# Kernel optimization log

Measured on AMD Instinct MI355X. Metric: run time of the kernel, lower is better.

Reference implementation:

```python
import jax, jax.numpy as jnp
import numpy as np

B, LINS, LHIS, LACT = 128, 64, 128, 32
VOCAB, ACTSZ = 2000, 100
INS_H, INS_E = 256, 128
ACT_E, ACT_IN, ACT_H = 128, 512, 512
POS_E, COL_E, COL_H = 32, 32, 32
ENV = 7 * (POS_E + COL_H)  # 448


def _lstm_cell(h, c, x, Wih, Whh, bih, bhh):
    # torch LSTM gate order: i, f, g, o
    g = x @ Wih.T + h @ Whh.T + bih + bhh
    i, f, gg, o = jnp.split(g, 4, axis=-1)
    c = jax.nn.sigmoid(f) * c + jax.nn.sigmoid(i) * jnp.tanh(gg)
    h = jax.nn.sigmoid(o) * jnp.tanh(c)
    return h, c


def _run_lstm(xs, Wih, Whh, bih, bhh):
    # xs: [T, N, D] -> hs: [T, N, H], zero initial state (torch default)
    N = xs.shape[1]
    H = Whh.shape[1]
    h0 = jnp.zeros((N, H), xs.dtype)

    def step(carry, x):
        h, c = carry
        h, c = _lstm_cell(h, c, x, Wih, Whh, bih, bhh)
        return (h, c), h

    _, hs = jax.lax.scan(step, (h0, h0), xs)
    return hs


def _bilstm_encode(tokens, emb, Wf, Uf, bf1, bf2, Wb, Ub, bb1, bb2):
    xs = emb[tokens].transpose(1, 0, 2)            # [L, B, E]
    hf = _run_lstm(xs, Wf, Uf, bf1, bf2)           # [L, B, H]
    hb = _run_lstm(xs[::-1], Wb, Ub, bb1, bb2)[::-1]
    return jnp.concatenate([hf, hb], -1).transpose(1, 0, 2)  # [B, L, 2H]


def _env_encode(tokens, color_emb, pos_emb, Wih, Whh, bih, bhh):
    # tokens: [B, 35] = 7 beakers x (id + 4 color slots)
    t = tokens.reshape(B, 7, 5)
    col = color_emb[t[:, :, 1:5]]                  # [B, 7, 4, COL_E]
    xs = col.reshape(B * 7, 4, COL_E).transpose(1, 0, 2)  # [4, B*7, COL_E]
    h_last = _run_lstm(xs, Wih, Whh, bih, bhh)[-1].reshape(B, 7, COL_H)
    pos = jnp.broadcast_to(pos_emb[None], (B, 7, POS_E))
    return jnp.concatenate([pos, h_last], -1).reshape(B, 7 * (POS_E + COL_H))


def _attend(A, H, q):
    # Faithful to attend(): scores = sum_k (H @ W)[b,l,k] * q[b,k]; softmax over l;
    # A = H @ W is query-independent so it is hoisted out of the decode loop.
    a = jax.nn.softmax(jnp.einsum('blk,bk->bl', A, q), axis=1)
    return jnp.einsum('bl,bld->bd', a, H)


def _forward(ins_tokens, his_tokens, actions, cur_env, ini_env,
             enc_emb, enc_Wih_f, enc_Whh_f, enc_bih_f, enc_bhh_f,
             enc_Wih_b, enc_Whh_b, enc_bih_b, enc_bhh_b,
             color_emb, pos_emb, ws_Wih, ws_Whh, ws_bih, ws_bhh,
             act_emb, W_c, W_p, W_sb1, W_sb2, W_sc1, W_sc2,
             Wbd_W, Wbd_b, dec_Wih, dec_Whh, dec_bih, dec_bhh,
             h2a_W, h2a_b, h0, c0):
    ins_enc = _bilstm_encode(ins_tokens, enc_emb, enc_Wih_f, enc_Whh_f, enc_bih_f,
                             enc_bhh_f, enc_Wih_b, enc_Whh_b, enc_bih_b, enc_bhh_b)
    his_enc = _bilstm_encode(his_tokens, enc_emb, enc_Wih_f, enc_Whh_f, enc_bih_f,
                             enc_bhh_f, enc_Wih_b, enc_Whh_b, enc_bih_b, enc_bhh_b)
    cur_ctx = _env_encode(cur_env, color_emb, pos_emb, ws_Wih, ws_Whh, ws_bih, ws_bhh)
    ini_ctx = _env_encode(ini_env, color_emb, pos_emb, ws_Wih, ws_Whh, ws_bih, ws_bhh)

    X = act_emb[actions]                            # [B, T, ACT_E]
    # Query-independent projections, hoisted out of the per-step loop (same math).
    A_c = jnp.einsum('bld,dk->blk', ins_enc, W_c)   # [B, LINS, ACT_H]
    A_p = jnp.einsum('bld,dk->blk', his_enc, W_p)   # [B, LHIS, ACT_H+2*INS_H]
    K = ACT_H + 2 * INS_H
    ini_rep = jnp.broadcast_to(ini_ctx[:, None, :], (B, LACT, ENV))
    cur_rep = jnp.broadcast_to(cur_ctx[:, None, :], (B, LACT, ENV))
    A_b1 = jnp.broadcast_to((ini_ctx @ W_sb1)[:, None, :], (B, LACT, K))
    A_b2 = jnp.broadcast_to((ini_ctx @ W_sb2)[:, None, :], (B, LACT, K))
    A_c1 = jnp.broadcast_to((cur_ctx @ W_sc1)[:, None, :], (B, LACT, K))
    A_c2 = jnp.broadcast_to((cur_ctx @ W_sc2)[:, None, :], (B, LACT, K))

    def step(carry, x_t):
        h, c = carry
        z_c = _attend(A_c, ins_enc, h)              # [B, 2*INS_H]
        q = jnp.concatenate([h, z_c], -1)           # [B, ACT_H+2*INS_H]
        z_p = _attend(A_p, his_enc, q)
        z_s1 = jnp.concatenate([_attend(A_b1, ini_rep, q),
                                _attend(A_b2, ini_rep, q)], -1)
        z_sk = jnp.concatenate([_attend(A_c1, cur_rep, q),
                                _attend(A_c2, cur_rep, q)], -1)
        hk1 = jnp.concatenate([z_c, z_p, z_s1, z_sk, x_t], -1)  # [B, 2944]
        hk = jnp.tanh(hk1 @ Wbd_W.T + Wbd_b)        # [B, ACT_IN]
        h, c = _lstm_cell(h, c, hk, dec_Wih, dec_Whh, dec_bih, dec_bhh)
        return (h, c), h

    _, outs = jax.lax.scan(step, (h0, c0), X.transpose(1, 0, 2))
    logits = outs.transpose(1, 0, 2) @ h2a_W.T + h2a_b  # [B, LACT, ACTSZ]
    return logits


def setup_inputs() -> dict:
    root = jax.random.key(0)
    ki = iter(jax.random.split(root, 40))

    def nrm(shape, s=0.05):
        return jax.random.normal(next(ki), shape, dtype=jnp.float32) * s

    inp = {}
    inp['ins_tokens'] = jax.random.randint(next(ki), (B, LINS), 0, VOCAB)
    inp['his_tokens'] = jax.random.randint(next(ki), (B, LHIS), 0, VOCAB)
    inp['actions'] = jax.random.randint(next(ki), (B, LACT), 0, ACTSZ)
    inp['cur_env'] = jax.random.randint(next(ki), (B, 35), 0, 7)
    inp['ini_env'] = jax.random.randint(next(ki), (B, 35), 0, 7)
    inp['enc_emb'] = nrm((VOCAB, INS_E))
    inp['enc_Wih_f'] = nrm((4 * INS_H, INS_E))
    inp['enc_Whh_f'] = nrm((4 * INS_H, INS_H))
    inp['enc_bih_f'] = nrm((4 * INS_H,))
    inp['enc_bhh_f'] = nrm((4 * INS_H,))
    inp['enc_Wih_b'] = nrm((4 * INS_H, INS_E))
    inp['enc_Whh_b'] = nrm((4 * INS_H, INS_H))
    inp['enc_bih_b'] = nrm((4 * INS_H,))
    inp['enc_bhh_b'] = nrm((4 * INS_H,))
    inp['color_emb'] = nrm((7, COL_E))
    inp['pos_emb'] = nrm((7, POS_E))
    inp['ws_Wih'] = nrm((4 * COL_H, COL_E))
    inp['ws_Whh'] = nrm((4 * COL_H, COL_H))
    inp['ws_bih'] = nrm((4 * COL_H,))
    inp['ws_bhh'] = nrm((4 * COL_H,))
    inp['act_emb'] = nrm((ACTSZ, ACT_E))
    inp['W_c'] = nrm((2 * INS_H, ACT_H))
    inp['W_p'] = nrm((2 * INS_H, 2 * INS_H + ACT_H))
    inp['W_sb1'] = nrm((ENV, ACT_H + 2 * INS_H))
    inp['W_sb2'] = nrm((ENV, ACT_H + 2 * INS_H))
    inp['W_sc1'] = nrm((ENV, ACT_H + 2 * INS_H))
    inp['W_sc2'] = nrm((ENV, ACT_H + 2 * INS_H))
    inp['Wbd_W'] = nrm((ACT_IN, 4 * ENV + 4 * INS_H + ACT_E))
    inp['Wbd_b'] = nrm((ACT_IN,))
    inp['dec_Wih'] = nrm((4 * ACT_H, ACT_IN))
    inp['dec_Whh'] = nrm((4 * ACT_H, ACT_H))
    inp['dec_bih'] = nrm((4 * ACT_H,))
    inp['dec_bhh'] = nrm((4 * ACT_H,))
    inp['h2a_W'] = nrm((ACTSZ, ACT_H))
    inp['h2a_b'] = nrm((ACTSZ,))
    inp['h0'] = nrm((B, ACT_H))
    inp['c0'] = nrm((B, ACT_H))
    return inp


def reference(ins_tokens, his_tokens, actions, cur_env, ini_env,
              enc_emb, enc_Wih_f, enc_Whh_f, enc_bih_f, enc_bhh_f,
              enc_Wih_b, enc_Whh_b, enc_bih_b, enc_bhh_b,
              color_emb, pos_emb, ws_Wih, ws_Whh, ws_bih, ws_bhh,
              act_emb, W_c, W_p, W_sb1, W_sb2, W_sc1, W_sc2,
              Wbd_W, Wbd_b, dec_Wih, dec_Whh, dec_bih, dec_bhh,
              h2a_W, h2a_b, h0, c0):
    return _forward(ins_tokens, his_tokens, actions, cur_env, ini_env,
                    enc_emb, enc_Wih_f, enc_Whh_f, enc_bih_f, enc_bhh_f,
                    enc_Wih_b, enc_Whh_b, enc_bih_b, enc_bhh_b,
                    color_emb, pos_emb, ws_Wih, ws_Whh, ws_bih, ws_bhh,
                    act_emb, W_c, W_p, W_sb1, W_sb2, W_sc1, W_sc2,
                    Wbd_W, Wbd_b, dec_Wih, dec_Whh, dec_bih, dec_bhh,
                    h2a_W, h2a_b, h0, c0)
```

## Files before the change

### kernel.cpp

```cpp
#include <hip/hip_runtime.h>


typedef unsigned short u16;
typedef __attribute__((ext_vector_type(8))) short bf16x8;
typedef __attribute__((ext_vector_type(4))) float f32x4;

#define DEVFN static __device__ __forceinline__

DEVFN float bf2f(u16 u) {
  unsigned int x = ((unsigned int)u) << 16;
  float f; __builtin_memcpy(&f, &x, 4); return f;
}
DEVFN u16 f2bf(float f) {
  unsigned int x; __builtin_memcpy(&x, &f, 4);
  x = (x + 0x7fffu + ((x >> 16) & 1u)) >> 16;
  return (u16)x;
}
DEVFN float sigf(float x) { return 1.f / (1.f + __expf(-x)); }
DEVFN bf16x8 load8(const u16* p) { return *(const bf16x8*)p; }
DEVFN int clampi(int v, int lo, int hi) { return v < lo ? lo : (v > hi ? hi : v); }

struct GemmArgs {
  const u16* A; int lda; int M;
  const u16* W; int ldw; int N; int K;
  void* out; int ldc;
  const float* bias;
  const float* hk_base; const float* proj_act; const int* actions; int t;
};

template <int EPI>
__global__ __launch_bounds__(256) void gemm_k(GemmArgs g) {
  int lane = threadIdx.x & 63;
  int wave = threadIdx.x >> 6;
  int col = lane & 15, q = lane >> 4;
  int m0 = blockIdx.x * 64 + (wave >> 1) * 32;
  int n0 = blockIdx.y * 64 + (wave & 1) * 32;
  f32x4 acc[2][2] = {};
  int rA[2] = { m0 + col, m0 + 16 + col };
  int rB[2] = { n0 + col, n0 + 16 + col };
  bool gA[2] = { rA[0] < g.M, rA[1] < g.M };
  bool gB[2] = { rB[0] < g.N, rB[1] < g.N };
  const u16* pA[2]; const u16* pB[2];
#pragma unroll
  for (int i = 0; i < 2; i++) {
    pA[i] = g.A + (size_t)(gA[i] ? rA[i] : 0) * g.lda + q * 8;
    pB[i] = g.W + (size_t)(gB[i] ? rB[i] : 0) * g.ldw + q * 8;
  }
  bf16x8 zf = {0,0,0,0,0,0,0,0};
  for (int k = 0; k < g.K; k += 32) {
    bf16x8 a0 = gA[0] ? load8(pA[0] + k) : zf;
    bf16x8 a1 = gA[1] ? load8(pA[1] + k) : zf;
    bf16x8 b0 = gB[0] ? load8(pB[0] + k) : zf;
    bf16x8 b1 = gB[1] ? load8(pB[1] + k) : zf;
    acc[0][0] = __builtin_amdgcn_mfma_f32_16x16x32_bf16(a0, b0, acc[0][0], 0, 0, 0);
    acc[0][1] = __builtin_amdgcn_mfma_f32_16x16x32_bf16(a0, b1, acc[0][1], 0, 0, 0);
    acc[1][0] = __builtin_amdgcn_mfma_f32_16x16x32_bf16(a1, b0, acc[1][0], 0, 0, 0);
    acc[1][1] = __builtin_amdgcn_mfma_f32_16x16x32_bf16(a1, b1, acc[1][1], 0, 0, 0);
  }
#pragma unroll
  for (int mi = 0; mi < 2; mi++)
#pragma unroll
    for (int ni = 0; ni < 2; ni++)
#pragma unroll
      for (int r = 0; r < 4; r++) {
        int m = m0 + mi * 16 + q * 4 + r;
        int n = n0 + ni * 16 + col;
        if (m >= g.M || n >= g.N) continue;
        float v = acc[mi][ni][r];
        if (g.bias) v += g.bias[n];
        ((float*)g.out)[(size_t)m * g.ldc + n] = v;
      }
}

template <int EPI>
__global__ __launch_bounds__(256) void gemm32_k(GemmArgs g) {
  int lane = threadIdx.x & 63;
  int wave = threadIdx.x >> 6;
  int col = lane & 15, q = lane >> 4;
  int m0 = blockIdx.x * 32 + (wave >> 1) * 16;
  int n0 = blockIdx.y * 32 + (wave & 1) * 16;
  f32x4 acc = {};
  int rA = m0 + col, rB = n0 + col;
  bool gA = rA < g.M, gB = rB < g.N;
  const u16* pA = g.A + (size_t)(gA ? rA : 0) * g.lda + q * 8;
  const u16* pB = g.W + (size_t)(gB ? rB : 0) * g.ldw + q * 8;
  bf16x8 zf = {0,0,0,0,0,0,0,0};
  for (int k = 0; k < g.K; k += 32) {
    bf16x8 a = gA ? load8(pA + k) : zf;
    bf16x8 b = gB ? load8(pB + k) : zf;
    acc = __builtin_amdgcn_mfma_f32_16x16x32_bf16(a, b, acc, 0, 0, 0);
  }
#pragma unroll
  for (int r = 0; r < 4; r++) {
    int m = m0 + q * 4 + r;
    int n = n0 + col;
    if (m >= g.M || n >= g.N) continue;
    float v = acc[r];
    if constexpr (EPI == 0) {
      if (g.bias) v += g.bias[n];
      ((float*)g.out)[(size_t)m * g.ldc + n] = v;
    } else {
      int act = clampi(g.actions[m * 32 + g.t], 0, 99);
      v += g.hk_base[m * 512 + n] + g.proj_act[(size_t)act * 512 + n];
      ((u16*)g.out)[(size_t)m * g.ldc + n] = f2bf(tanhf(v));
    }
  }
}

__global__ __launch_bounds__(256) void dec_gates_cell32(
    const u16* zin_cur, const u16* Wih, const u16* Whh, const float* bias_int,
    float* c_ws, u16* zin_nxt, u16* qbuf, u16* outs, int t) {
  int lane = threadIdx.x & 63, wave = threadIdx.x >> 6;
  int col = lane & 15, q = lane >> 4;
  int m0 = blockIdx.x * 32 + (wave >> 1) * 16;
  int n0 = blockIdx.y * 32 + (wave & 1) * 16;
  f32x4 acc = {};
  const u16* pA = zin_cur + (size_t)(m0 + col) * 1024 + q * 8;
  int r = n0 + col;
  int src = (r & 3) * 512 + (r >> 2);
  const u16* pI = Wih + (size_t)src * 512 + q * 8;
  const u16* pH = Whh + (size_t)src * 512 + q * 8;
  for (int k = 0; k < 512; k += 32) {
    acc = __builtin_amdgcn_mfma_f32_16x16x32_bf16(load8(pA + k), load8(pI + k), acc, 0, 0, 0);
  }
  for (int k = 0; k < 512; k += 32) {
    acc = __builtin_amdgcn_mfma_f32_16x16x32_bf16(load8(pA + 512 + k), load8(pH + k), acc, 0, 0, 0);
  }
  __shared__ float ls[32][36];
#pragma unroll
  for (int rr = 0; rr < 4; rr++) {
    int ml = (wave >> 1) * 16 + q * 4 + rr;
    int nl = (wave & 1) * 16 + col;
    ls[ml][nl] = acc[rr] + bias_int[blockIdx.y * 32 + nl];
  }
  __syncthreads();
  int m = threadIdx.x & 31, jloc = threadIdx.x >> 5;
  int gm = blockIdx.x * 32 + m;
  int j = blockIdx.y * 8 + jloc;
  float gi = ls[m][jloc * 4 + 0];
  float gf = ls[m][jloc * 4 + 1];
  float gg = ls[m][jloc * 4 + 2];
  float go = ls[m][jloc * 4 + 3];
  float cn = sigf(gf) * c_ws[gm * 512 + j] + sigf(gi) * tanhf(gg);
  c_ws[gm * 512 + j] = cn;
  float hn = sigf(go) * tanhf(cn);
  u16 hb = f2bf(hn);
  zin_nxt[(size_t)gm * 1024 + 512 + j] = hb;
  qbuf[(size_t)gm * 1024 + j] = hb;
  outs[((size_t)gm * 32 + t) * 512 + j] = hb;
}

struct CvtJob { const float* src; u16* dst; int R; int C; int ld; int c0; int tr; int blk0; };
struct CvtJobs { CvtJob j[15]; int njobs; };

__global__ void cvt_all(CvtJobs a) {
  int bid = blockIdx.x;
  int ji = 0;
  while (ji + 1 < a.njobs && bid >= a.j[ji + 1].blk0) ji++;
  CvtJob jb = a.j[ji];
  int idx = (bid - jb.blk0) * 256 + threadIdx.x;
  int n = jb.R * jb.C;
  if (idx >= n) return;
  int r = idx / jb.C, c = idx - r * jb.C;
  float v = jb.src[(size_t)r * jb.ld + jb.c0 + c];
  if (jb.tr) jb.dst[(size_t)c * jb.R + r] = f2bf(v);
  else jb.dst[idx] = f2bf(v);
}

__global__ void addcvt(const float* a, const float* b, float* o, int n) {
  int i = blockIdx.x * 256 + threadIdx.x;
  if (i < n) o[i] = a[i] + (b ? b[i] : 0.f);
}

__global__ void bdecint_build(const float* bih, const float* bhh, float* o) {
  int r = blockIdx.x * 256 + threadIdx.x;
  int j = r >> 2, gg = r & 3;
  o[r] = bih[gg * 512 + j] + bhh[gg * 512 + j];
}

__global__ void wsum_build(const float* Wbd, u16* Wsum) {
  int idx = blockIdx.x * 256 + threadIdx.x;
  int n = idx / 896, j = idx % 896;
  int c1 = (j < 448) ? (1024 + j) : (1920 + (j - 448));
  int c2 = c1 + 448;
  Wsum[idx] = f2bf(Wbd[(size_t)n * 2944 + c1] + Wbd[(size_t)n * 2944 + c2]);
}

__global__ __launch_bounds__(256) void env_encode(
    const int* cur_env, const int* ini_env,
    const float* color_emb, const float* pos_emb,
    const float* wih, const float* whh, const float* bih, const float* bhh,
    u16* ctx_cat) {
  __shared__ float s_wih[128 * 33], s_whh[128 * 33], s_b[128], s_col[7 * 32];
  __shared__ float h_lds[8][33];
  int tid = threadIdx.x;
  for (int i = tid; i < 128 * 32; i += 256) {
    int r = i >> 5, k2 = i & 31;
    s_wih[r * 33 + k2] = wih[i];
    s_whh[r * 33 + k2] = whh[i];
  }
  for (int i = tid; i < 128; i += 256) s_b[i] = bih[i] + bhh[i];
  for (int i = tid; i < 224; i += 256) s_col[i] = color_emb[i];
  int sl = tid >> 5, j = tid & 31;
  int gseq = blockIdx.x * 8 + sl;
  int e = gseq / 896, rem = gseq % 896;
  int b = rem / 7, p = rem % 7;
  const int* env = e ? ini_env : cur_env;
  int eoff = e ? 0 : 448;
  h_lds[sl][j] = 0.f;
  __syncthreads();
  float cj = 0.f, hj = 0.f;
  for (int st = 0; st < 4; st++) {
    int tok = clampi(env[b * 35 + p * 5 + 1 + st], 0, 6);
    const float* x = &s_col[tok * 32];
    float pi = s_b[j], pf = s_b[32 + j], pg = s_b[64 + j], po = s_b[96 + j];
    for (int k = 0; k < 32; k++) {
      float xk = x[k], hk = h_lds[sl][k];
      pi += s_wih[j * 33 + k] * xk + s_whh[j * 33 + k] * hk;
      pf += s_wih[(32 + j) * 33 + k] * xk + s_whh[(32 + j) * 33 + k] * hk;
      pg += s_wih[(64 + j) * 33 + k] * xk + s_whh[(64 + j) * 33 + k] * hk;
      po += s_wih[(96 + j) * 33 + k] * xk + s_whh[(96 + j) * 33 + k] * hk;
    }
    cj = sigf(pf) * cj + sigf(pi) * tanhf(pg);
    hj = sigf(po) * tanhf(cj);
    __syncthreads();
    h_lds[sl][j] = hj;
    __syncthreads();
  }
  size_t base = (size_t)b * 896 + eoff + p * 64;
  ctx_cat[base + j] = f2bf(pos_emb[p * 32 + j]);
  ctx_cat[base + 32 + j] = f2bf(hj);
}

#define HBUF ((size_t)4 * 128 * 256)
__global__ __launch_bounds__(256) void enc_step2(
    int t, int chainbase,
    const int* ins_tok, const int* his_tok,
    const float* projE_f, const float* projE_b,
    const u16* whh_f, const u16* whh_b,
    const float* bias_f, const float* bias_b,
    u16* h_enc, float* c_enc,
    u16* ins_enc, u16* his_enc) {
  int chain = chainbase + (blockIdx.x >> 5);
  int sub = blockIdx.x & 31;
  int sgrp = sub >> 2, jq = sub & 3;
  int w = threadIdx.x >> 6, lane = threadIdx.x & 63;
  int col = lane & 15, q = lane >> 4;
  int dir = chain & 1, his = chain >> 1;
  int L = his ? 128 : 64;
  const int* toks = his ? his_tok : ins_tok;
  int t_x = dir ? (L - 1 - t) : t;
  const float* projE = dir ? projE_b : projE_f;
  const u16* whh = dir ? whh_b : whh_f;
  const float* bias = dir ? bias_b : bias_f;
  const u16* h_rd = h_enc + ((size_t)((t & 1) ^ 1)) * HBUF + (size_t)chain * 128 * 256;
  u16* h_wr = h_enc + ((size_t)(t & 1)) * HBUF + (size_t)chain * 128 * 256;
  float* c_g = c_enc + (size_t)chain * 128 * 256;
  u16* out = his ? his_enc : ins_enc;

  int jw = jq * 64 + w * 16;
  f32x4 acc[4] = {};
  if (t > 0) {
    const u16* hrow = h_rd + (size_t)(sgrp * 16 + col) * 256 + q * 8;
    const u16* wrow[4];
#pragma unroll
    for (int G = 0; G < 4; G++) wrow[G] = whh + (size_t)(G * 256 + jw + col) * 256 + q * 8;
    for (int k = 0; k < 256; k += 32) {
      bf16x8 a = load8(hrow + k);
#pragma unroll
      for (int G = 0; G < 4; G++) {
        bf16x8 bb = load8(wrow[G] + k);
        acc[G] = __builtin_amdgcn_mfma_f32_16x16x32_bf16(a, bb, acc[G], 0, 0, 0);
      }
    }
  }
  int j = jw + col;
  float bi = bias[j], bf = bias[256 + j], bg = bias[512 + j], bo = bias[768 + j];
#pragma unroll
  for (int r = 0; r < 4; r++) {
    int s = q * 4 + r;
    int b = sgrp * 16 + s;
    int tok = clampi(toks[b * L + t_x], 0, 1999);
    const float* px = projE + (size_t)tok * 1024;
    float pi = acc[0][r] + px[j] + bi;
    float pf = acc[1][r] + px[256 + j] + bf;
    float pg = acc[2][r] + px[512 + j] + bg;
    float po = acc[3][r] + px[768 + j] + bo;
    float cold = (t > 0) ? c_g[b * 256 + j] : 0.f;
    float cn = sigf(pf) * cold + sigf(pi) * tanhf(pg);
    float hn = sigf(po) * tanhf(cn);
    c_g[b * 256 + j] = cn;
    u16 hb = f2bf(hn);
    h_wr[b * 256 + j] = hb;
    out[((size_t)b * L + t_x) * 512 + dir * 256 + j] = hb;
  }
}

__global__ __launch_bounds__(256) void attn1(
    const float* u_c, const u16* insenc, u16* qattn, u16* qbuf) {
  int b = blockIdx.x, tid = threadIdx.x;
  __shared__ float su[512], red[256], aw[64];
  __shared__ float zacc[4][512];
  for (int d = tid; d < 512; d += 256) su[d] = u_c[b * 512 + d];
  __syncthreads();
  {
    int l = tid >> 2, part = tid & 3;
    const u16* row = insenc + ((size_t)b * 64 + l) * 512 + part * 128;
    float s = 0.f;
    for (int k = 0; k < 128; k += 8) {
      bf16x8 v = load8(row + k);
#pragma unroll
      for (int e = 0; e < 8; e++) s += bf2f((u16)v[e]) * su[part * 128 + k + e];
    }
    red[tid] = s;
  }
  __syncthreads();
  if (tid < 64) {
    float sc = red[tid * 4] + red[tid * 4 + 1] + red[tid * 4 + 2] + red[tid * 4 + 3];
    float m = sc;
    for (int off = 32; off > 0; off >>= 1) m = fmaxf(m, __shfl_xor(m, off));
    float e = __expf(sc - m);
    float sm = e;
    for (int off = 32; off > 0; off >>= 1) sm += __shfl_xor(sm, off);
    aw[tid] = e / sm;
  }
  __syncthreads();
  {
    int part = tid >> 6, chunk = tid & 63;
    float a[8] = {};
    for (int l = part * 16; l < part * 16 + 16; l++) {
      bf16x8 v = load8(insenc + ((size_t)b * 64 + l) * 512 + chunk * 8);
      float w = aw[l];
#pragma unroll
      for (int e = 0; e < 8; e++) a[e] += w * bf2f((u16)v[e]);
    }
#pragma unroll
    for (int e = 0; e < 8; e++) zacc[part][chunk * 8 + e] = a[e];
  }
  __syncthreads();
  for (int d = tid; d < 512; d += 256) {
    float z = zacc[0][d] + zacc[1][d] + zacc[2][d] + zacc[3][d];
    u16 zb = f2bf(z);
    qattn[(size_t)b * 1024 + d] = zb;
    qbuf[(size_t)b * 1024 + 512 + d] = zb;
  }
}

__global__ __launch_bounds__(256) void attn2(
    const float* u_p, const u16* hisenc, u16* qattn) {
  int b = blockIdx.x, tid = threadIdx.x;
  __shared__ float su[512], red[256], aw[128], mr[2];
  __shared__ float zacc[4][512];
  for (int d = tid; d < 512; d += 256) su[d] = u_p[b * 512 + d];
  __syncthreads();
  {
    int l = tid >> 1, part = tid & 1;
    const u16* row = hisenc + ((size_t)b * 128 + l) * 512 + part * 256;
    float s = 0.f;
    for (int k = 0; k < 256; k += 8) {
      bf16x8 v = load8(row + k);
#pragma unroll
      for (int e = 0; e < 8; e++) s += bf2f((u16)v[e]) * su[part * 256 + k + e];
    }
    red[tid] = s;
  }
  __syncthreads();
  float sc = (tid < 128) ? red[tid * 2] + red[tid * 2 + 1] : 0.f;
  __syncthreads();
  if (tid < 128) red[tid] = sc;
  __syncthreads();
  if (tid < 64) {
    float m = fmaxf(red[tid], red[tid + 64]);
    for (int off = 32; off > 0; off >>= 1) m = fmaxf(m, __shfl_xor(m, off));
    if (tid == 0) mr[0] = m;
  }
  __syncthreads();
  float ex = 0.f;
  if (tid < 128) { ex = __expf(sc - mr[0]); red[tid] = ex; }
  __syncthreads();
  if (tid < 64) {
    float s2 = red[tid] + red[tid + 64];
    for (int off = 32; off > 0; off >>= 1) s2 += __shfl_xor(s2, off);
    if (tid == 0) mr[1] = s2;
  }
  __syncthreads();
  if (tid < 128) aw[tid] = ex / mr[1];
  __syncthreads();
  {
    int part = tid >> 6, chunk = tid & 63;
    float a[8] = {};
    for (int l = part * 32; l < part * 32 + 32; l++) {
      bf16x8 v = load8(hisenc + ((size_t)b * 128 + l) * 512 + chunk * 8);
      float w = aw[l];
#pragma unroll
      for (int e = 0; e < 8; e++) a[e] += w * bf2f((u16)v[e]);
    }
#pragma unroll
    for (int e = 0; e < 8; e++) zacc[part][chunk * 8 + e] = a[e];
  }
  __syncthreads();
  for (int d = tid; d < 512; d += 256) {
    float z = zacc[0][d] + zacc[1][d] + zacc[2][d] + zacc[3][d];
    qattn[(size_t)b * 1024 + 512 + d] = f2bf(z);
  }
}

__global__ void dec_init(const float* h0, const float* c0, u16* zin0, u16* qbuf, float* c_ws) {
  int idx = blockIdx.x * 256 + threadIdx.x;
  int b = idx >> 9, d = idx & 511;
  u16 hv = f2bf(h0[idx]);
  zin0[(size_t)b * 1024 + 512 + d] = hv;
  qbuf[(size_t)b * 1024 + d] = hv;
  c_ws[idx] = c0[idx];
}

extern "C" void kernel_launch(void* const* d_in, const int* in_sizes, int n_in,
                              void* d_out, int out_size, void* d_ws, size_t ws_size,
                              hipStream_t stream) {
  const int* ins_tok = (const int*)d_in[0];
  const int* his_tok = (const int*)d_in[1];
  const int* actions = (const int*)d_in[2];
  const int* cur_env = (const int*)d_in[3];
  const int* ini_env = (const int*)d_in[4];
  const float* enc_emb = (const float*)d_in[5];
  const float* Wih_f = (const float*)d_in[6];
  const float* Whh_f = (const float*)d_in[7];
  const float* bih_f = (const float*)d_in[8];
  const float* bhh_f = (const float*)d_in[9];
  const float* Wih_b = (const float*)d_in[10];
  const float* Whh_b = (const float*)d_in[11];
  const float* bih_b = (const float*)d_in[12];
  const float* bhh_b = (const float*)d_in[13];
  const float* color_emb = (const float*)d_in[14];
  const float* pos_emb = (const float*)d_in[15];
  const float* ws_Wih = (const float*)d_in[16];
  const float* ws_Whh = (const float*)d_in[17];
  const float* ws_bih = (const float*)d_in[18];
  const float* ws_bhh = (const float*)d_in[19];
  const float* act_emb = (const float*)d_in[20];
  const float* W_c = (const float*)d_in[21];
  const float* W_p = (const float*)d_in[22];
  const float* Wbd_W = (const float*)d_in[27];
  const float* Wbd_b = (const float*)d_in[28];
  const float* dec_Wih = (const float*)d_in[29];
  const float* dec_Whh = (const float*)d_in[30];
  const float* dec_bih = (const float*)d_in[31];
  const float* dec_bhh = (const float*)d_in[32];
  const float* h2a_W = (const float*)d_in[33];
  const float* h2a_b = (const float*)d_in[34];
  const float* h0 = (const float*)d_in[35];
  const float* c0 = (const float*)d_in[36];
  (void)in_sizes; (void)n_in; (void)out_size; (void)ws_size;

  char* ws = (char*)d_ws;
  size_t off = 0;
  auto alloc = [&](size_t bytes) -> char* {
    char* p = ws + off;
    off = (off + bytes + 255) & ~(size_t)255;
    return p;
  };
  u16* insenc   = (u16*)alloc(8192ull * 512 * 2);
  u16* hisenc   = (u16*)alloc(16384ull * 512 * 2);
  u16* outs     = (u16*)alloc(4096ull * 512 * 2);
  u16* Wsum     = (u16*)alloc(512ull * 896 * 2);
  u16* h_enc    = (u16*)alloc(2 * HBUF * 2);
  float* c_enc  = (float*)alloc(4ull * 128 * 256 * 4);
  float* projact= (float*)alloc(100ull * 512 * 4);
  float* bias_f = (float*)alloc(1024 * 4);
  float* bias_b = (float*)alloc(1024 * 4);
  float* bdecint= (float*)alloc(2048 * 4);
  float* bwbd   = (float*)alloc(512 * 4);
  float* bh2a   = (float*)alloc(128 * 4);
  u16* ctxcat   = (u16*)alloc(128ull * 896 * 2);
  float* hkbase = (float*)alloc(128ull * 512 * 4);
  float* u_c    = (float*)alloc(128ull * 512 * 4);
  float* u_p    = (float*)alloc(128ull * 512 * 4);
  u16* qbuf     = (u16*)alloc(128ull * 1024 * 2);
  u16* qattn    = (u16*)alloc(128ull * 1024 * 2);
  u16* zin      = (u16*)alloc(2ull * 128 * 1024 * 2);
  float* c_dec  = (float*)alloc(128ull * 512 * 4);
  float* projE_f = (float*)alloc(2000ull * 1024 * 4);
  float* projE_b = (float*)alloc(2000ull * 1024 * 4);
  u16* emb_bf   = (u16*)alloc(2000ull * 128 * 2);
  u16* wihf_bf  = (u16*)alloc(1024ull * 128 * 2);
  u16* wihb_bf  = (u16*)alloc(1024ull * 128 * 2);
  u16* whhf_bf  = (u16*)alloc(1024ull * 256 * 2);
  u16* whhb_bf  = (u16*)alloc(1024ull * 256 * 2);
  u16* act_bf   = (u16*)alloc(100ull * 128 * 2);
  u16* wc_bf    = (u16*)alloc(512ull * 512 * 2);
  u16* wp_bf    = (u16*)alloc(512ull * 1024 * 2);
  u16* wbd01_bf = (u16*)alloc(512ull * 1024 * 2);
  u16* wbdx_bf  = (u16*)alloc(512ull * 128 * 2);
  u16* dwih_bf  = (u16*)alloc(2048ull * 512 * 2);
  u16* dwhh_bf  = (u16*)alloc(2048ull * 512 * 2);
  u16* h2a_bf   = (u16*)alloc(100ull * 512 * 2);

  CvtJobs cj{};
  int nb = 0, jn = 0;
  auto addjob = [&](const float* s, u16* d, int R, int C, int ld, int c0c, int tr) {
    cj.j[jn] = { s, d, R, C, ld, c0c, tr, nb };
    nb += (R * C + 255) / 256;
    jn++;
  };
  addjob(enc_emb, emb_bf, 2000, 128, 128, 0, 0);
  addjob(Wih_f, wihf_bf, 1024, 128, 128, 0, 0);
  addjob(Wih_b, wihb_bf, 1024, 128, 128, 0, 0);
  addjob(Whh_f, whhf_bf, 1024, 256, 256, 0, 0);
  addjob(Whh_b, whhb_bf, 1024, 256, 256, 0, 0);
  addjob(act_emb, act_bf, 100, 128, 128, 0, 0);
  addjob(W_c, wc_bf, 512, 512, 512, 0, 0);
  addjob(W_p, wp_bf, 512, 1024, 1024, 0, 0);
  addjob(Wbd_W, wbd01_bf, 512, 1024, 2944, 0, 0);
  addjob(Wbd_W, wbdx_bf, 512, 128, 2944, 2816, 0);
  addjob(dec_Wih, dwih_bf, 2048, 512, 512, 0, 0);
  addjob(dec_Whh, dwhh_bf, 2048, 512, 512, 0, 0);
  addjob(h2a_W, h2a_bf, 100, 512, 512, 0, 0);
  cj.njobs = jn;
  cvt_all<<<nb, 256, 0, stream>>>(cj);

  addcvt<<<4, 256, 0, stream>>>(bih_f, bhh_f, bias_f, 1024);
  addcvt<<<4, 256, 0, stream>>>(bih_b, bhh_b, bias_b, 1024);
  addcvt<<<2, 256, 0, stream>>>(Wbd_b, nullptr, bwbd, 512);
  addcvt<<<1, 256, 0, stream>>>(h2a_b, nullptr, bh2a, 100);
  bdecint_build<<<8, 256, 0, stream>>>(dec_bih, dec_bhh, bdecint);
  wsum_build<<<1792, 256, 0, stream>>>(Wbd_W, Wsum);

  {
    GemmArgs ge = {};
    ge.A = emb_bf; ge.lda = 128; ge.M = 2000; ge.W = wihf_bf; ge.ldw = 128;
    ge.N = 1024; ge.K = 128; ge.out = projE_f; ge.ldc = 1024;
    gemm_k<0><<<dim3(32, 16), 256, 0, stream>>>(ge);
    ge.W = wihb_bf; ge.out = projE_b;
    gemm_k<0><<<dim3(32, 16), 256, 0, stream>>>(ge);
  }

  GemmArgs gp = {};
  gp.A = act_bf; gp.lda = 128; gp.M = 100; gp.W = wbdx_bf; gp.ldw = 128;
  gp.N = 512; gp.K = 128; gp.out = projact; gp.ldc = 512; gp.bias = bwbd;
  gemm_k<0><<<dim3(2, 8), 256, 0, stream>>>(gp);

  env_encode<<<224, 256, 0, stream>>>(cur_env, ini_env, color_emb, pos_emb,
                                      ws_Wih, ws_Whh, ws_bih, ws_bhh, ctxcat);
  GemmArgs gb = {};
  gb.A = ctxcat; gb.lda = 896; gb.M = 128; gb.W = Wsum; gb.ldw = 896;
  gb.N = 512; gb.K = 896; gb.out = hkbase; gb.ldc = 512;
  gemm_k<0><<<dim3(2, 8), 256, 0, stream>>>(gb);

  for (int t = 0; t < 128; t++) {
    int cb = (t < 64) ? 0 : 2;
    int nbk = (t < 64) ? 128 : 64;
    enc_step2<<<nbk, 256, 0, stream>>>(t, cb, ins_tok, his_tok,
                                       projE_f, projE_b, whhf_bf, whhb_bf,
                                       bias_f, bias_b, h_enc, c_enc,
                                       insenc, hisenc);
  }

  dec_init<<<256, 256, 0, stream>>>(h0, c0, zin, qbuf, c_dec);
  for (int t = 0; t < 32; t++) {
    u16* zin_cur = zin + (size_t)(t & 1) * 128 * 1024;
    u16* zin_nxt = zin + (size_t)((t + 1) & 1) * 128 * 1024;
    GemmArgs gu = {};
    gu.A = qbuf; gu.lda = 1024; gu.M = 128; gu.W = wc_bf; gu.ldw = 512;
    gu.N = 512; gu.K = 512; gu.out = u_c; gu.ldc = 512;
    gemm32_k<0><<<dim3(4, 16), 256, 0, stream>>>(gu);
    attn1<<<128, 256, 0, stream>>>(u_c, insenc, qattn, qbuf);
    GemmArgs gv = {};
    gv.A = qbuf; gv.lda = 1024; gv.M = 128; gv.W = wp_bf; gv.ldw = 1024;
    gv.N = 512; gv.K = 1024; gv.out = u_p; gv.ldc = 512;
    gemm32_k<0><<<dim3(4, 16), 256, 0, stream>>>(gv);
    attn2<<<128, 256, 0, stream>>>(u_p, hisenc, qattn);
    GemmArgs gh = {};
    gh.A = qattn; gh.lda = 1024; gh.M = 128; gh.W = wbd01_bf; gh.ldw = 1024;
    gh.N = 512; gh.K = 1024; gh.out = zin_cur; gh.ldc = 1024;
    gh.hk_base = hkbase; gh.proj_act = projact; gh.actions = actions; gh.t = t;
    gemm32_k<2><<<dim3(4, 16), 256, 0, stream>>>(gh);
    dec_gates_cell32<<<dim3(4, 64), 256, 0, stream>>>(
        zin_cur, dwih_bf, dwhh_bf, bdecint, c_dec, zin_nxt, qbuf, outs, t);
  }

  GemmArgs gl = {};
  gl.A = outs; gl.lda = 512; gl.M = 4096; gl.W = h2a_bf; gl.ldw = 512;
  gl.N = 100; gl.K = 512; gl.out = d_out; gl.ldc = 100; gl.bias = bh2a;
  gemm32_k<0><<<dim3(128, 4), 256, 0, stream>>>(gl);
}
```

Before: 3.127 ms.

## Precompute attention keys H·W_c once and split encoder step into smaller blocks

Instead of projecting the query through W_c on every decode step, the instruction encoder outputs are multiplied by W_c once after encoding (a large 8192x512x512 GEMM into bf16), and attn1 dots the raw query against these precomputed keys. This removes one GEMM launch per decode step but adds a big one-time GEMM and a bf16 rounding of the keys. The encoder step kernel is also rebuilt with 128-thread blocks and twice as many blocks, and five small bias-prep launches are merged into one.

```diff
diff --git a/kernel.cpp b/kernel.cpp
--- a/kernel.cpp
+++ b/kernel.cpp
@@ -67,8 +67,12 @@
         int n = n0 + ni * 16 + col;
         if (m >= g.M || n >= g.N) continue;
         float v = acc[mi][ni][r];
-        if (g.bias) v += g.bias[n];
-        ((float*)g.out)[(size_t)m * g.ldc + n] = v;
+        if constexpr (EPI == 0) {
+          if (g.bias) v += g.bias[n];
+          ((float*)g.out)[(size_t)m * g.ldc + n] = v;
+        } else {
+          ((u16*)g.out)[(size_t)m * g.ldc + n] = f2bf(v);
+        }
       }
 }
 
@@ -167,15 +171,22 @@
   else jb.dst[idx] = f2bf(v);
 }
 
-__global__ void addcvt(const float* a, const float* b, float* o, int n) {
+__global__ void prep_small(
+    const float* bih_f, const float* bhh_f, float* bias_f,
+    const float* bih_b, const float* bhh_b, float* bias_b,
+    const float* Wbd_b, float* bwbd,
+    const float* h2a_b, float* bh2a,
+    const float* dec_bih, const float* dec_bhh, float* bdecint) {
   int i = blockIdx.x * 256 + threadIdx.x;
-  if (i < n) o[i] = a[i] + (b ? b[i] : 0.f);
-}
-
-__global__ void bdecint_build(const float* bih, const float* bhh, float* o) {
-  int r = blockIdx.x * 256 + threadIdx.x;
-  int j = r >> 2, gg = r & 3;
-  o[r] = bih[gg * 512 + j] + bhh[gg * 512 + j];
+  if (i < 1024) bias_f[i] = bih_f[i] + bhh_f[i];
+  else if (i < 2048) { int k = i - 1024; bias_b[k] = bih_b[k] + bhh_b[k]; }
+  else if (i < 2560) { int k = i - 2048; bwbd[k] = Wbd_b[k]; }
+  else if (i < 2660) { int k = i - 2560; bh2a[k] = h2a_b[k]; }
+  else if (i < 4708) {
+    int r = i - 2660;
+    int j = r >> 2, gg = r & 3;
+    bdecint[r] = dec_bih[gg * 512 + j] + dec_bhh[gg * 512 + j];
+  }
 }
 
 __global__ void wsum_build(const float* Wbd, u16* Wsum) {
@@ -233,7 +244,7 @@
 }
 
 #define HBUF ((size_t)4 * 128 * 256)
-__global__ __launch_bounds__(256) void enc_step2(
+__global__ __launch_bounds__(128) void enc_step3(
     int t, int chainbase,
     const int* ins_tok, const int* his_tok,
     const float* projE_f, const float* projE_b,
@@ -241,9 +252,9 @@
     const float* bias_f, const float* bias_b,
     u16* h_enc, float* c_enc,
     u16* ins_enc, u16* his_enc) {
-  int chain = chainbase + (blockIdx.x >> 5);
-  int sub = blockIdx.x & 31;
-  int sgrp = sub >> 2, jq = sub & 3;
+  int chain = chainbase + (blockIdx.x >> 6);
+  int sub = blockIdx.x & 63;
+  int sgrp = sub >> 3, jq = sub & 7;
   int w = threadIdx.x >> 6, lane = threadIdx.x & 63;
   int col = lane & 15, q = lane >> 4;
   int dir = chain & 1, his = chain >> 1;
@@ -258,7 +269,7 @@
   float* c_g = c_enc + (size_t)chain * 128 * 256;
   u16* out = his ? his_enc : ins_enc;
 
-  int jw = jq * 64 + w * 16;
+  int jw = jq * 32 + w * 16;
   f32x4 acc[4] = {};
   if (t > 0) {
     const u16* hrow = h_rd + (size_t)(sgrp * 16 + col) * 256 + q * 8;
@@ -297,15 +308,15 @@
 }
 
 __global__ __launch_bounds__(256) void attn1(
-    const float* u_c, const u16* insenc, u16* qattn, u16* qbuf) {
+    const u16* A_c, const u16* insenc, u16* qattn, u16* qbuf) {
   int b = blockIdx.x, tid = threadIdx.x;
   __shared__ float su[512], red[256], aw[64];
   __shared__ float zacc[4][512];
-  for (int d = tid; d < 512; d += 256) su[d] = u_c[b * 512 + d];
+  for (int d = tid; d < 512; d += 256) su[d] = bf2f(qbuf[(size_t)b * 1024 + d]);
   __syncthreads();
   {
     int l = tid >> 2, part = tid & 3;
-    const u16* row = insenc + ((size_t)b * 64 + l) * 512 + part * 128;
+    const u16* row = A_c + ((size_t)b * 64 + l) * 512 + part * 128;
     float s = 0.f;
     for (int k = 0; k < 128; k += 8) {
       bf16x8 v = load8(row + k);
@@ -473,7 +484,6 @@
   float* bh2a   = (float*)alloc(128 * 4);
   u16* ctxcat   = (u16*)alloc(128ull * 896 * 2);
   float* hkbase = (float*)alloc(128ull * 512 * 4);
-  float* u_c    = (float*)alloc(128ull * 512 * 4);
   float* u_p    = (float*)alloc(128ull * 512 * 4);
   u16* qbuf     = (u16*)alloc(128ull * 1024 * 2);
   u16* qattn    = (u16*)alloc(128ull * 1024 * 2);
@@ -481,13 +491,14 @@
   float* c_dec  = (float*)alloc(128ull * 512 * 4);
   float* projE_f = (float*)alloc(2000ull * 1024 * 4);
   float* projE_b = (float*)alloc(2000ull * 1024 * 4);
+  u16* A_c      = (u16*)alloc(8192ull * 512 * 2);
   u16* emb_bf   = (u16*)alloc(2000ull * 128 * 2);
   u16* wihf_bf  = (u16*)alloc(1024ull * 128 * 2);
   u16* wihb_bf  = (u16*)alloc(1024ull * 128 * 2);
   u16* whhf_bf  = (u16*)alloc(1024ull * 256 * 2);
   u16* whhb_bf  = (u16*)alloc(1024ull * 256 * 2);
   u16* act_bf   = (u16*)alloc(100ull * 128 * 2);
-  u16* wc_bf    = (u16*)alloc(512ull * 512 * 2);
+  u16* wcT_bf   = (u16*)alloc(512ull * 512 * 2);
   u16* wp_bf    = (u16*)alloc(512ull * 1024 * 2);
   u16* wbd01_bf = (u16*)alloc(512ull * 1024 * 2);
   u16* wbdx_bf  = (u16*)alloc(512ull * 128 * 2);
@@ -508,7 +519,7 @@
   addjob(Whh_f, whhf_bf, 1024, 256, 256, 0, 0);
   addjob(Whh_b, whhb_bf, 1024, 256, 256, 0, 0);
   addjob(act_emb, act_bf, 100, 128, 128, 0, 0);
-  addjob(W_c, wc_bf, 512, 512, 512, 0, 0);
+  addjob(W_c, wcT_bf, 512, 512, 512, 0, 1);
   addjob(W_p, wp_bf, 512, 1024, 1024, 0, 0);
   addjob(Wbd_W, wbd01_bf, 512, 1024, 2944, 0, 0);
   addjob(Wbd_W, wbdx_bf, 512, 128, 2944, 2816, 0);
@@ -518,11 +529,9 @@
   cj.njobs = jn;
   cvt_all<<<nb, 256, 0, stream>>>(cj);
 
-  addcvt<<<4, 256, 0, stream>>>(bih_f, bhh_f, bias_f, 1024);
-  addcvt<<<4, 256, 0, stream>>>(bih_b, bhh_b, bias_b, 1024);
-  addcvt<<<2, 256, 0, stream>>>(Wbd_b, nullptr, bwbd, 512);
-  addcvt<<<1, 256, 0, stream>>>(h2a_b, nullptr, bh2a, 100);
-  bdecint_build<<<8, 256, 0, stream>>>(dec_bih, dec_bhh, bdecint);
+  prep_small<<<19, 256, 0, stream>>>(bih_f, bhh_f, bias_f, bih_b, bhh_b, bias_b,
+                                     Wbd_b, bwbd, h2a_b, bh2a,
+                                     dec_bih, dec_bhh, bdecint);
   wsum_build<<<1792, 256, 0, stream>>>(Wbd_W, Wsum);
 
   {
@@ -548,22 +557,25 @@
 
   for (int t = 0; t < 128; t++) {
     int cb = (t < 64) ? 0 : 2;
-    int nbk = (t < 64) ? 128 : 64;
-    enc_step2<<<nbk, 256, 0, stream>>>(t, cb, ins_tok, his_tok,
+    int nbk = (t < 64) ? 256 : 128;
+    enc_step3<<<nbk, 128, 0, stream>>>(t, cb, ins_tok, his_tok,
                                        projE_f, projE_b, whhf_bf, whhb_bf,
                                        bias_f, bias_b, h_enc, c_enc,
                                        insenc, hisenc);
+  }
+
+  {
+    GemmArgs ga = {};
+    ga.A = insenc; ga.lda = 512; ga.M = 8192; ga.W = wcT_bf; ga.ldw = 512;
+    ga.N = 512; ga.K = 512; ga.out = A_c; ga.ldc = 512;
+    gemm_k<1><<<dim3(128, 8), 256, 0, stream>>>(ga);
   }
 
   dec_init<<<256, 256, 0, stream>>>(h0, c0, zin, qbuf, c_dec);
   for (int t = 0; t < 32; t++) {
     u16* zin_cur = zin + (size_t)(t & 1) * 128 * 1024;
     u16* zin_nxt = zin + (size_t)((t + 1) & 1) * 128 * 1024;
-    GemmArgs gu = {};
-    gu.A = qbuf; gu.lda = 1024; gu.M = 128; gu.W = wc_bf; gu.ldw = 512;
-    gu.N = 512; gu.K = 512; gu.out = u_c; gu.ldc = 512;
-    gemm32_k<0><<<dim3(4, 16), 256, 0, stream>>>(gu);
-    attn1<<<128, 256, 0, stream>>>(u_c, insenc, qattn, qbuf);
+    attn1<<<128, 256, 0, stream>>>(A_c, insenc, qattn, qbuf);
     GemmArgs gv = {};
     gv.A = qbuf; gv.lda = 1024; gv.M = 128; gv.W = wp_bf; gv.ldw = 1024;
     gv.N = 512; gv.K = 1024; gv.out = u_p; gv.ldc = 512;
```

Result: faster. 2.716 ms (-13.2%).
